# Kernel tuning notes

Hardware: AMD Instinct MI355X
Metric: run time of the kernel (lower is better)

## Reference

```python
import jax, jax.numpy as jnp
import numpy as np
from jax import lax

TEMPERATURE = 0.0005


def conv1d(x, w, b, pad):
    # x: [B, Cin, T], w: [Cout, Cin, K], b: [Cout]
    y = lax.conv_general_dilated(x, w, window_strides=(1,), padding=[(pad, pad)],
                                 dimension_numbers=('NCH', 'OIH', 'NCH'))
    return y + b[None, :, None]


def setup_inputs() -> dict:
    key = jax.random.key(0)
    ks = jax.random.split(key, 16)
    B, Cq, Ck, Ca, Tde, Ten = 32, 80, 512, 80, 2000, 400

    def xavier(k, shape):
        fan_in = shape[1] * (shape[2] if len(shape) > 2 else 1)
        fan_out = shape[0] * (shape[2] if len(shape) > 2 else 1)
        lim = float(np.sqrt(6.0 / (fan_in + fan_out)))
        return jax.random.uniform(k, shape, jnp.float32, -lim, lim)

    inp = {
        'queries': jax.random.normal(ks[0], (B, Cq, Tde), jnp.float32),
        'keys': jax.random.normal(ks[1], (B, Ck, Ten), jnp.float32),
        'mask': jnp.ones((B, 1, Ten), jnp.int32),
        # key_layer: Conv(512->1024,k3,p1) -> ReLU -> Conv(1024->80,k1)
        'kw1': xavier(ks[2], (Ck * 2, Ck, 3)), 'kb1': jnp.zeros((Ck * 2,), jnp.float32),
        'kw2': xavier(ks[3], (Ca, Ck * 2, 1)), 'kb2': jnp.zeros((Ca,), jnp.float32),
        # query_layer: Conv(80->160,k3,p1)->ReLU->Conv(160->80,k1)->ReLU->Conv(80->80,k1)
        'qw1': xavier(ks[4], (Cq * 2, Cq, 3)), 'qb1': jnp.zeros((Cq * 2,), jnp.float32),
        'qw2': xavier(ks[5], (Cq, Cq * 2, 1)), 'qb2': jnp.zeros((Cq,), jnp.float32),
        'qw3': xavier(ks[6], (Ca, Cq, 1)), 'qb3': jnp.zeros((Ca,), jnp.float32),
    }
    return inp


def reference(queries, keys, mask, kw1, kb1, kw2, kb2, qw1, qb1, qw2, qb2, qw3, qb3):
    # key path: conv3 -> relu -> conv1
    k = conv1d(jax.nn.relu(conv1d(keys, kw1, kb1, 1)), kw2, kb2, 0)          # [B,Ca,Ten]
    # query path: conv3 -> relu -> conv1 -> relu -> conv1
    q = conv1d(queries, qw1, qb1, 1)
    q = jax.nn.relu(conv1d(jax.nn.relu(q), qw2, qb2, 0))
    q = conv1d(q, qw3, qb3, 0)                                               # [B,Ca,Tde]

    # sum_c (q - k)^2 = |q|^2 + |k|^2 - 2 q.k  (avoids [B,C,Tde,Ten] intermediate)
    q2 = jnp.sum(q * q, axis=1)                      # [B,Tde]
    k2 = jnp.sum(k * k, axis=1)                      # [B,Ten]
    qk = jnp.einsum('bcd,bce->bde', q, k)            # [B,Tde,Ten]
    dist = q2[:, :, None] + k2[:, None, :] - 2.0 * qk
    attn_logp = (-TEMPERATURE * dist)[:, None]       # [B,1,Tde,Ten]

    # masked fill over encoder positions (softmax dim)
    m = mask.astype(bool)[:, :, None, :]             # [B,1,1,Ten]
    attn_logp = jnp.where(m, attn_logp, -jnp.inf)
    attn = jax.nn.softmax(attn_logp, axis=3)
    return attn, attn_logp
```

## Files before the change

### kernel.cpp

```cpp
#include <hip/hip_runtime.h>
#include <hip/hip_bf16.h>
#include <math.h>

#define NB 32
#define CK 512
#define C1 1024
#define CA 80
#define CQ 80
#define CQ2 160
#define TEN 400
#define TDE 2000
#define KDIM 1536
#define TPAD 448
#define TQP 2048

static constexpr float TEMP = 0.0005f;

typedef __attribute__((ext_vector_type(8))) short short8;
typedef __attribute__((ext_vector_type(4))) float f32x4;

__device__ inline short f2bf(float v) {
  __hip_bfloat16 h = __float2bfloat16(v);
  return *(short*)&h;
}

__device__ inline void gload_lds16(const void* g, void* l) {
  __builtin_amdgcn_global_load_lds(
      (const __attribute__((address_space(1))) unsigned int*)g,
      (__attribute__((address_space(3))) unsigned int*)l, 16, 0, 0);
}

__global__ __launch_bounds__(256) void cvt_w1_kernel(
    const float* __restrict__ w1, short* __restrict__ w1bf) {
  int i = blockIdx.x * 256 + threadIdx.x;
  if (i < C1 * KDIM) w1bf[i] = f2bf(w1[i]);
}

__global__ __launch_bounds__(256) void cvt_pad_kernel(
    const float* __restrict__ src, short* __restrict__ dst,
    int M, int K, int Mp, int Kp) {
  int i = blockIdx.x * 256 + threadIdx.x;
  if (i >= Mp * Kp) return;
  int r = i / Kp, c = i - r * Kp;
  float v = (r < M && c < K) ? src[(size_t)r * K + c] : 0.f;
  dst[i] = f2bf(v);
}

__global__ __launch_bounds__(256) void im2col_kernel(
    const float* __restrict__ keys, short* __restrict__ BmatT) {
  const int t = blockIdx.x;
  const int b = blockIdx.y;
  const int tid = threadIdx.x;
  short* dst = BmatT + ((size_t)b * TPAD + t) * KDIM;
  #pragma unroll
  for (int i = 0; i < 6; ++i) {
    int k = tid + i * 256;
    int ci = k / 3;
    int dk = k - ci * 3;
    int ts = t + dk - 1;
    float v = (ts >= 0 && ts < TEN) ? keys[((size_t)b * CK + ci) * TEN + ts] : 0.f;
    dst[k] = f2bf(v);
  }
}

__global__ __launch_bounds__(256) void im2col_q_kernel(
    const float* __restrict__ queries, short* __restrict__ Bq) {
  const int t = blockIdx.x;
  const int b = blockIdx.y;
  const int k = threadIdx.x;
  float v = 0.f;
  if (t < TDE && k < 240) {
    int ci = k / 3, dk = k - ci * 3, ts = t + dk - 1;
    v = (ts >= 0 && ts < TDE) ? queries[((size_t)b * CQ + ci) * TDE + ts] : 0.f;
  }
  Bq[((size_t)b * TQP + t) * 256 + k] = f2bf(v);
}

__global__ __launch_bounds__(256) void kconv1_mfma_kernel(
    const short* __restrict__ w1bf, const short* __restrict__ BmatT,
    const float* __restrict__ b1, short* __restrict__ k1t) {
  __shared__ short A_lds[4096];
  __shared__ short B_lds[2048];
  const int co0 = blockIdx.x * 128;
  const int t0  = blockIdx.y * 64;
  const int b   = blockIdx.z;
  const int tid = threadIdx.x;
  const int l = tid & 63, w = tid >> 6;

  auto invswz = [](int Y) {
    int X = Y;
    X ^= ((Y >> 8) & 1) << 6;
    X ^= ((Y >> 7) & 1) << 5;
    X ^= (((Y >> 6) ^ (Y >> 8)) & 1) << 4;
    return X;
  };

  const short* gA[2];
  #pragma unroll
  for (int c = 0; c < 2; ++c) {
    int Y = (w * 2 + c) * 1024 + l * 16;
    int X = invswz(Y);
    int row = X >> 6, slot = (X >> 4) & 3;
    gA[c] = w1bf + (size_t)(co0 + row) * KDIM + slot * 8;
  }
  const short* gB;
  {
    int Y = w * 1024 + l * 16;
    int X = invswz(Y);
    int row = X >> 6, slot = (X >> 4) & 3;
    gB = BmatT + ((size_t)b * TPAD + t0 + row) * KDIM + slot * 8;
  }
  short* ldsA0 = &A_lds[(w * 2 + 0) * 512];
  short* ldsA1 = &A_lds[(w * 2 + 1) * 512];
  short* ldsB  = &B_lds[w * 512];

  const int kslot = l >> 4;
  int abyte[2];
  #pragma unroll
  for (int i = 0; i < 2; ++i) {
    int arow = w * 32 + i * 16 + (l & 15);
    abyte[i] = (arow * 64 + kslot * 16) ^ ((arow & 7) << 4);
  }
  int bbyte[4];
  #pragma unroll
  for (int g = 0; g < 4; ++g) {
    int brow = g * 16 + (l & 15);
    bbyte[g] = (brow * 64 + kslot * 16) ^ ((brow & 7) << 4);
  }

  f32x4 acc[2][4];
  #pragma unroll
  for (int i = 0; i < 2; ++i)
    #pragma unroll
    for (int g = 0; g < 4; ++g) acc[i][g] = (f32x4){0.f, 0.f, 0.f, 0.f};

  for (int kt = 0; kt < KDIM / 32; ++kt) {
    __syncthreads();
    gload_lds16(gA[0] + kt * 32, ldsA0);
    gload_lds16(gA[1] + kt * 32, ldsA1);
    gload_lds16(gB + kt * 32, ldsB);
    __syncthreads();
    short8 a0 = *(const short8*)((const char*)A_lds + abyte[0]);
    short8 a1 = *(const short8*)((const char*)A_lds + abyte[1]);
    #pragma unroll
    for (int g = 0; g < 4; ++g) {
      short8 bb = *(const short8*)((const char*)B_lds + bbyte[g]);
      acc[0][g] = __builtin_amdgcn_mfma_f32_16x16x32_bf16(a0, bb, acc[0][g], 0, 0, 0);
      acc[1][g] = __builtin_amdgcn_mfma_f32_16x16x32_bf16(a1, bb, acc[1][g], 0, 0, 0);
    }
  }

  #pragma unroll
  for (int g = 0; g < 4; ++g) {
    int t = t0 + g * 16 + (l & 15);
    if (t < TEN) {
      #pragma unroll
      for (int i = 0; i < 2; ++i) {
        #pragma unroll
        for (int r = 0; r < 4; ++r) {
          int co = co0 + w * 32 + i * 16 + kslot * 4 + r;
          float v = acc[i][g][r] + b1[co];
          k1t[((size_t)b * TPAD + t) * C1 + co] = f2bf(v > 0.f ? v : 0.f);
        }
      }
    }
  }
}

template <int MODE, bool RELU>
__global__ __launch_bounds__(256) void qgemm_kernel(
    const short* __restrict__ A, const short* __restrict__ B,
    const float* __restrict__ bias, void* __restrict__ outv,
    int M, int Kpad, int kiters, int Nvalid, int outCols,
    size_t bBatchStride, size_t outBatchStride, int outLD) {
  __shared__ short A_lds[2048];
  __shared__ short B_lds[2048];
  const int co0 = blockIdx.x * 64;
  const int t0  = blockIdx.y * 64;
  const int b   = blockIdx.z;
  const int tid = threadIdx.x;
  const int l = tid & 63, w = tid >> 6;
  const int srow = tid >> 2, sslot = tid & 3;

  const short* gA = A + (size_t)(co0 + srow) * Kpad + sslot * 8;
  const short* gB = B + (size_t)b * bBatchStride + (size_t)(t0 + srow) * Kpad + sslot * 8;
  const int wbyte = (srow * 64 + sslot * 16) ^ ((srow & 7) << 4);

  const int kslot = l >> 4;
  const int arow = w * 16 + (l & 15);
  const int abyte = (arow * 64 + kslot * 16) ^ ((arow & 7) << 4);
  int bbyte[4];
  #pragma unroll
  for (int g = 0; g < 4; ++g) {
    int brow = g * 16 + (l & 15);
    bbyte[g] = (brow * 64 + kslot * 16) ^ ((brow & 7) << 4);
  }

  f32x4 acc[4];
  #pragma unroll
  for (int g = 0; g < 4; ++g) acc[g] = (f32x4){0.f, 0.f, 0.f, 0.f};

  uint4 av = *(const uint4*)gA;
  uint4 bv = *(const uint4*)gB;
  for (int kt = 0; kt < kiters; ++kt) {
    __syncthreads();
    *(uint4*)((char*)A_lds + wbyte) = av;
    *(uint4*)((char*)B_lds + wbyte) = bv;
    __syncthreads();
    uint4 an = av, bn = bv;
    if (kt + 1 < kiters) {
      an = *(const uint4*)(gA + (kt + 1) * 32);
      bn = *(const uint4*)(gB + (kt + 1) * 32);
    }
    short8 a = *(const short8*)((const char*)A_lds + abyte);
    #pragma unroll
    for (int g = 0; g < 4; ++g) {
      short8 bb = *(const short8*)((const char*)B_lds + bbyte[g]);
      acc[g] = __builtin_amdgcn_mfma_f32_16x16x32_bf16(a, bb, acc[g], 0, 0, 0);
    }
    av = an; bv = bn;
  }

  #pragma unroll
  for (int g = 0; g < 4; ++g) {
    int t = t0 + g * 16 + (l & 15);
    if (t >= Nvalid) continue;
    #pragma unroll
    for (int r = 0; r < 4; ++r) {
      int co = co0 + w * 16 + kslot * 4 + r;
      if (MODE == 1) {
        if (co < outCols) {
          float v = 0.f;
          if (co < M) {
            v = acc[g][r] + bias[co];
            if (RELU) v = v > 0.f ? v : 0.f;
          }
          ((short*)outv)[(size_t)b * outBatchStride + (size_t)t * outLD + co] = f2bf(v);
        }
      } else {
        if (co < M) {
          float v = acc[g][r] + bias[co];
          if (RELU) v = v > 0.f ? v : 0.f;
          ((float*)outv)[(size_t)b * outBatchStride + (size_t)co * outLD + t] = v;
        }
      }
    }
  }
}

__global__ __launch_bounds__(256) void prep_attn_q_kernel(
    const float* __restrict__ q3, short* __restrict__ qA,
    float* __restrict__ q2) {
  __shared__ float sm[80][64];
  const int b = blockIdx.y;
  const int t0 = blockIdx.x * 64;
  const int tid = threadIdx.x;
  for (int idx = tid; idx < 80 * 64; idx += 256) {
    int a = idx >> 6, j = idx & 63;
    int t = t0 + j;
    sm[a][j] = (t < TDE) ? q3[((size_t)b * CA + a) * TDE + t] : 0.f;
  }
  __syncthreads();
  if (tid < 64) {
    float ss = 0.f;
    #pragma unroll 8
    for (int a = 0; a < 80; ++a) { float v = sm[a][tid]; ss += v * v; }
    q2[(size_t)b * TQP + t0 + tid] = ss;
  }
  for (int idx = tid; idx < 64 * 96; idx += 256) {
    int j = idx / 96, k = idx - j * 96;
    float v = (k < 80) ? sm[k][j] : 0.f;
    qA[((size_t)b * TQP + t0 + j) * 96 + k] = f2bf(v);
  }
}

__global__ __launch_bounds__(256) void prep_attn_k_kernel(
    const float* __restrict__ kfeat, short* __restrict__ kB,
    float* __restrict__ k2) {
  __shared__ float sm[80][64];
  const int b = blockIdx.y;
  const int s0 = blockIdx.x * 64;
  const int tid = threadIdx.x;
  for (int idx = tid; idx < 80 * 64; idx += 256) {
    int a = idx >> 6, j = idx & 63;
    int s = s0 + j;
    sm[a][j] = (s < TEN) ? kfeat[((size_t)b * CA + a) * TEN + s] : 0.f;
  }
  __syncthreads();
  if (tid < 64) {
    float ss = 0.f;
    #pragma unroll 8
    for (int a = 0; a < 80; ++a) { float v = sm[a][tid]; ss += v * v; }
    k2[(size_t)b * TPAD + s0 + tid] = ss;
  }
  for (int idx = tid; idx < 64 * 96; idx += 256) {
    int j = idx / 96, k = idx - j * 96;
    float v = (k < 80) ? sm[k][j] : 0.f;
    kB[((size_t)b * TPAD + s0 + j) * 96 + k] = f2bf(v);
  }
}

__global__ __launch_bounds__(256) void attn_fused_kernel(
    const short* __restrict__ qA, const short* __restrict__ kB,
    const float* __restrict__ q2, const float* __restrict__ k2,
    const int* __restrict__ mask, float* __restrict__ out_attn,
    float* __restrict__ out_logp) {
  __shared__ short A_lds[3][2048];
  __shared__ short B_lds[3][2560];
  __shared__ float k2LDS[400];
  __shared__ int mLDS[400];
  const int t0 = blockIdx.x * 64;
  const int b  = blockIdx.y;
  const int tid = threadIdx.x;
  const int l = tid & 63, w = tid >> 6;

  {
    const int arow_s = tid >> 2, aslot = tid & 3;
    const short* gA = qA + ((size_t)b * TQP + t0 + arow_s) * 96 + aslot * 8;
    #pragma unroll
    for (int p = 0; p < 3; ++p) {
      uint4 v = *(const uint4*)(gA + p * 32);
      *(uint4*)((char*)&A_lds[p][0] +
                ((arow_s * 64 + aslot * 16) ^ ((arow_s & 7) << 4))) = v;
    }
  }
  for (int idx = tid; idx < 400; idx += 256) {
    k2LDS[idx] = k2[(size_t)b * TPAD + idx];
    mLDS[idx] = mask[(size_t)b * TEN + idx];
  }

  const int kslot = l >> 4;
  const int arow = w * 16 + (l & 15);
  const int abyte = (arow * 64 + kslot * 16) ^ ((arow & 7) << 4);

  f32x4 acc[25];
  #pragma unroll
  for (int i = 0; i < 25; ++i) acc[i] = (f32x4){0.f, 0.f, 0.f, 0.f};

  __syncthreads();
  #pragma unroll
  for (int st = 0; st < 5; ++st) {
    for (int idx = tid; idx < 960; idx += 256) {
      int row = idx / 12, c = idx - row * 12;
      int panel = c >> 2, ps = c & 3;
      uint4 v = *(const uint4*)(kB + ((size_t)b * TPAD + st * 80 + row) * 96 + c * 8);
      *(uint4*)((char*)&B_lds[panel][0] +
                ((row * 64 + ps * 16) ^ ((row & 7) << 4))) = v;
    }
    __syncthreads();
    #pragma unroll
    for (int kt = 0; kt < 3; ++kt) {
      short8 a = *(const short8*)((const char*)&A_lds[kt][0] + abyte);
      #pragma unroll
      for (int f = 0; f < 5; ++f) {
        int brow = f * 16 + (l & 15);
        short8 bb = *(const short8*)((const char*)&B_lds[kt][0] +
                                     ((brow * 64 + kslot * 16) ^ ((brow & 7) << 4)));
        acc[st * 5 + f] =
            __builtin_amdgcn_mfma_f32_16x16x32_bf16(a, bb, acc[st * 5 + f], 0, 0, 0);
      }
    }
    __syncthreads();
  }

  int trow[4]; float q2v[4];
  #pragma unroll
  for (int r = 0; r < 4; ++r) {
    trow[r] = t0 + w * 16 + kslot * 4 + r;
    q2v[r] = q2[(size_t)b * TQP + trow[r]];
  }
  #pragma unroll
  for (int sf = 0; sf < 25; ++sf) {
    int s = sf * 16 + (l & 15);
    float k2v = k2LDS[s];
    bool mk = mLDS[s] != 0;
    #pragma unroll
    for (int r = 0; r < 4; ++r) {
      float lp = mk ? (-TEMP) * (q2v[r] + k2v - 2.f * acc[sf][r]) : -INFINITY;
      acc[sf][r] = lp;
    }
  }
  #pragma unroll
  for (int r = 0; r < 4; ++r) {
    if (trow[r] < TDE) {
      float* dst = out_logp + ((size_t)(b * TDE + trow[r])) * TEN + (l & 15);
      #pragma unroll
      for (int sf = 0; sf < 25; ++sf) dst[sf * 16] = acc[sf][r];
    }
  }
  float m[4];
  #pragma unroll
  for (int r = 0; r < 4; ++r) m[r] = -INFINITY;
  #pragma unroll
  for (int sf = 0; sf < 25; ++sf)
    #pragma unroll
    for (int r = 0; r < 4; ++r) m[r] = fmaxf(m[r], acc[sf][r]);
  #pragma unroll
  for (int o = 1; o < 16; o <<= 1)
    #pragma unroll
    for (int r = 0; r < 4; ++r) m[r] = fmaxf(m[r], __shfl_xor(m[r], o, 64));
  float sum[4] = {0.f, 0.f, 0.f, 0.f};
  #pragma unroll
  for (int sf = 0; sf < 25; ++sf)
    #pragma unroll
    for (int r = 0; r < 4; ++r) {
      float v = acc[sf][r];
      float e = (v != -INFINITY) ? __expf(v - m[r]) : 0.f;
      acc[sf][r] = e;
      sum[r] += e;
    }
  #pragma unroll
  for (int o = 1; o < 16; o <<= 1)
    #pragma unroll
    for (int r = 0; r < 4; ++r) sum[r] += __shfl_xor(sum[r], o, 64);
  float inv[4];
  #pragma unroll
  for (int r = 0; r < 4; ++r) inv[r] = 1.0f / sum[r];
  #pragma unroll
  for (int r = 0; r < 4; ++r) {
    if (trow[r] < TDE) {
      float* dst = out_attn + ((size_t)(b * TDE + trow[r])) * TEN + (l & 15);
      #pragma unroll
      for (int sf = 0; sf < 25; ++sf) dst[sf * 16] = acc[sf][r] * inv[r];
    }
  }
}

extern "C" void kernel_launch(void* const* d_in, const int* in_sizes, int n_in,
                              void* d_out, int out_size, void* d_ws, size_t ws_size,
                              hipStream_t stream) {
  const float* queries = (const float*)d_in[0];
  const float* keys    = (const float*)d_in[1];
  const int*   mask    = (const int*)d_in[2];
  const float* kw1 = (const float*)d_in[3];
  const float* kb1 = (const float*)d_in[4];
  const float* kw2 = (const float*)d_in[5];
  const float* kb2 = (const float*)d_in[6];
  const float* qw1 = (const float*)d_in[7];
  const float* qb1 = (const float*)d_in[8];
  const float* qw2 = (const float*)d_in[9];
  const float* qb2 = (const float*)d_in[10];
  const float* qw3 = (const float*)d_in[11];
  const float* qb3 = (const float*)d_in[12];
  float* out = (float*)d_out;

  char* ws = (char*)d_ws;
  short* BmatT = (short*)ws;
  short* w1bf  = (short*)(ws + 44040192);
  short* k1t   = (short*)(ws + 47185920);
  short* w2bf  = (short*)(ws + 76546048);
  short* w1q   = (short*)(ws + 76808192);
  short* w2q   = (short*)(ws + 76906496);
  short* w3q   = (short*)(ws + 76947456);
  short* Bq    = (short*)ws;
  short* q1bf  = (short*)(ws + 33554432);
  short* q2bf  = (short*)(ws + 54525952);
  float* q3    = (float*)ws;
  short* qA    = (short*)(ws + 20480000);
  float* q2n   = (float*)(ws + 33062912);
  short* kB    = (short*)(ws + 47185920);
  float* k2n   = (float*)(ws + 49938432);
  float* kfeat = (float*)(ws + 81920000);

  const long long HALF = 25600000LL;
  float* out_attn = out;
  float* out_logp = out + HALF;

  cvt_w1_kernel<<<dim3((C1 * KDIM + 255) / 256), dim3(256), 0, stream>>>(kw1, w1bf);
  im2col_kernel<<<dim3(TEN, NB), dim3(256), 0, stream>>>(keys, BmatT);
  kconv1_mfma_kernel<<<dim3(8, 7, NB), dim3(256), 0, stream>>>(w1bf, BmatT, kb1, k1t);
  cvt_pad_kernel<<<dim3((128 * 1024 + 255) / 256), dim3(256), 0, stream>>>(
      kw2, w2bf, CA, C1, 128, C1);
  qgemm_kernel<2, false><<<dim3(2, 7, NB), dim3(256), 0, stream>>>(
      w2bf, k1t, kb2, kfeat, CA, C1, 32, TEN, CA,
      (size_t)TPAD * C1, (size_t)CA * TEN, TEN);

  cvt_pad_kernel<<<dim3((192 * 256 + 255) / 256), dim3(256), 0, stream>>>(
      qw1, w1q, CQ2, 240, 192, 256);
  cvt_pad_kernel<<<dim3((128 * 160 + 255) / 256), dim3(256), 0, stream>>>(
      qw2, w2q, CA, CQ2, 128, 160);
  cvt_pad_kernel<<<dim3((128 * 96 + 255) / 256), dim3(256), 0, stream>>>(
      qw3, w3q, CA, CQ, 128, 96);
  im2col_q_kernel<<<dim3(TQP, NB), dim3(256), 0, stream>>>(queries, Bq);
  qgemm_kernel<1, true><<<dim3(3, TQP / 64, NB), dim3(256), 0, stream>>>(
      w1q, Bq, qb1, q1bf, CQ2, 256, 8, TDE, 160,
      (size_t)TQP * 256, (size_t)TQP * 160, 160);
  qgemm_kernel<1, true><<<dim3(2, TQP / 64, NB), dim3(256), 0, stream>>>(
      w2q, q1bf, qb2, q2bf, CA, 160, 5, TDE, 96,
      (size_t)TQP * 160, (size_t)TQP * 96, 96);
  qgemm_kernel<2, false><<<dim3(2, TQP / 64, NB), dim3(256), 0, stream>>>(
      w3q, q2bf, qb3, q3, CA, 96, 3, TDE, 80,
      (size_t)TQP * 96, (size_t)CA * TDE, TDE);

  prep_attn_q_kernel<<<dim3(TQP / 64, NB), dim3(256), 0, stream>>>(q3, qA, q2n);
  prep_attn_k_kernel<<<dim3(TPAD / 64, NB), dim3(256), 0, stream>>>(kfeat, kB, k2n);
  attn_fused_kernel<<<dim3(TQP / 64, NB), dim3(256), 0, stream>>>(
      qA, kB, q2n, k2n, mask, out_attn, out_logp);
}
```

Measured before the change: 380.0 us.

## Widen key conv1 MFMA tile to 128 time steps and flatten grid

```diff
diff --git a/kernel.cpp b/kernel.cpp
--- a/kernel.cpp
+++ b/kernel.cpp
@@ -80,10 +80,14 @@
     const short* __restrict__ w1bf, const short* __restrict__ BmatT,
     const float* __restrict__ b1, short* __restrict__ k1t) {
   __shared__ short A_lds[4096];
-  __shared__ short B_lds[2048];
-  const int co0 = blockIdx.x * 128;
-  const int t0  = blockIdx.y * 64;
-  const int b   = blockIdx.z;
+  __shared__ short B_lds[4096];
+  const int flat = blockIdx.x;
+  const int cox = flat >> 7;
+  const int rem = flat & 127;
+  const int b   = rem >> 2;
+  const int ty  = rem & 3;
+  const int co0 = cox * 128;
+  const int t0  = ty * 128;
   const int tid = threadIdx.x;
   const int l = tid & 63, w = tid >> 6;
 
@@ -95,24 +99,24 @@
     return X;
   };
 
-  const short* gA[2];
-  #pragma unroll
-  for (int c = 0; c < 2; ++c) {
-    int Y = (w * 2 + c) * 1024 + l * 16;
+  const short* gsrc[4];
+  short* ldst[4];
+  #pragma unroll
+  for (int j = 0; j < 4; ++j) {
+    int c = w * 4 + j;
+    int Y = (c & 7) * 1024 + l * 16;
     int X = invswz(Y);
     int row = X >> 6, slot = (X >> 4) & 3;
-    gA[c] = w1bf + (size_t)(co0 + row) * KDIM + slot * 8;
-  }
-  const short* gB;
-  {
-    int Y = w * 1024 + l * 16;
-    int X = invswz(Y);
-    int row = X >> 6, slot = (X >> 4) & 3;
-    gB = BmatT + ((size_t)b * TPAD + t0 + row) * KDIM + slot * 8;
-  }
-  short* ldsA0 = &A_lds[(w * 2 + 0) * 512];
-  short* ldsA1 = &A_lds[(w * 2 + 1) * 512];
-  short* ldsB  = &B_lds[w * 512];
+    if (c < 8) {
+      gsrc[j] = w1bf + (size_t)(co0 + row) * KDIM + slot * 8;
+      ldst[j] = &A_lds[(c & 7) * 512];
+    } else {
+      int gr = t0 + row;
+      if (gr > TPAD - 1) gr = TPAD - 1;
+      gsrc[j] = BmatT + ((size_t)b * TPAD + gr) * KDIM + slot * 8;
+      ldst[j] = &B_lds[(c & 7) * 512];
+    }
+  }
 
   const int kslot = l >> 4;
   int abyte[2];
@@ -121,29 +125,28 @@
     int arow = w * 32 + i * 16 + (l & 15);
     abyte[i] = (arow * 64 + kslot * 16) ^ ((arow & 7) << 4);
   }
-  int bbyte[4];
-  #pragma unroll
-  for (int g = 0; g < 4; ++g) {
+  int bbyte[8];
+  #pragma unroll
+  for (int g = 0; g < 8; ++g) {
     int brow = g * 16 + (l & 15);
     bbyte[g] = (brow * 64 + kslot * 16) ^ ((brow & 7) << 4);
   }
 
-  f32x4 acc[2][4];
+  f32x4 acc[2][8];
   #pragma unroll
   for (int i = 0; i < 2; ++i)
     #pragma unroll
-    for (int g = 0; g < 4; ++g) acc[i][g] = (f32x4){0.f, 0.f, 0.f, 0.f};
+    for (int g = 0; g < 8; ++g) acc[i][g] = (f32x4){0.f, 0.f, 0.f, 0.f};
 
   for (int kt = 0; kt < KDIM / 32; ++kt) {
     __syncthreads();
-    gload_lds16(gA[0] + kt * 32, ldsA0);
-    gload_lds16(gA[1] + kt * 32, ldsA1);
-    gload_lds16(gB + kt * 32, ldsB);
+    #pragma unroll
+    for (int j = 0; j < 4; ++j) gload_lds16(gsrc[j] + kt * 32, ldst[j]);
     __syncthreads();
     short8 a0 = *(const short8*)((const char*)A_lds + abyte[0]);
     short8 a1 = *(const short8*)((const char*)A_lds + abyte[1]);
     #pragma unroll
-    for (int g = 0; g < 4; ++g) {
+    for (int g = 0; g < 8; ++g) {
       short8 bb = *(const short8*)((const char*)B_lds + bbyte[g]);
       acc[0][g] = __builtin_amdgcn_mfma_f32_16x16x32_bf16(a0, bb, acc[0][g], 0, 0, 0);
       acc[1][g] = __builtin_amdgcn_mfma_f32_16x16x32_bf16(a1, bb, acc[1][g], 0, 0, 0);
@@ -151,7 +154,7 @@
   }
 
   #pragma unroll
-  for (int g = 0; g < 4; ++g) {
+  for (int g = 0; g < 8; ++g) {
     int t = t0 + g * 16 + (l & 15);
     if (t < TEN) {
       #pragma unroll
@@ -468,7 +471,7 @@
 
   cvt_w1_kernel<<<dim3((C1 * KDIM + 255) / 256), dim3(256), 0, stream>>>(kw1, w1bf);
   im2col_kernel<<<dim3(TEN, NB), dim3(256), 0, stream>>>(keys, BmatT);
-  kconv1_mfma_kernel<<<dim3(8, 7, NB), dim3(256), 0, stream>>>(w1bf, BmatT, kb1, k1t);
+  kconv1_mfma_kernel<<<dim3(1024), dim3(256), 0, stream>>>(w1bf, BmatT, kb1, k1t);
   cvt_pad_kernel<<<dim3((128 * 1024 + 255) / 256), dim3(256), 0, stream>>>(
       kw2, w2bf, CA, C1, 128, C1);
   qgemm_kernel<2, false><<<dim3(2, 7, NB), dim3(256), 0, stream>>>(
```

New measurement: 370.3 us. 1.03x faster.
